# Performance work log

Measured on AMD Instinct MI355X. Metric: run time of the kernel, lower is better.

## Reference

```python
import jax, jax.numpy as jnp
import numpy as np

D_MODEL = 1024
N_HEADS = 16
KV_HEADS = 4
D_HEAD = D_MODEL // N_HEADS


def _rope_factor(n, d_head, dtype):
    # theta = 10000 ** (-2*(i//2)/d_head); buffers cos/sin = outer(pos, theta)
    # then sin[1::2] (odd positions) negated. Module applies q*cos + q*sin,
    # i.e. elementwise scale by (cos + sin_mod) -- faithful to the source.
    i = jnp.arange(d_head)
    theta = jnp.power(jnp.asarray(10000.0, dtype), (-2.0 * (i // 2) / d_head).astype(dtype))
    pos = jnp.arange(n, dtype=dtype)
    ang = pos[:, None] * theta[None, :]          # [n, d_head]
    sign = jnp.where(jnp.arange(n) % 2 == 1, -1.0, 1.0).astype(dtype)
    return jnp.cos(ang) + sign[:, None] * jnp.sin(ang)  # [n, d_head]


def _rms_norm(x, g):
    eps = jnp.finfo(x.dtype).eps  # torch nn.RMSNorm(eps=None) default
    inv = jax.lax.rsqrt(jnp.mean(x * x, axis=-1, keepdims=True) + eps)
    return x * inv * g


def setup_inputs() -> dict:
    key = jax.random.key(0)
    ks = jax.random.split(key, 5)
    s_in = 1.0 / np.sqrt(D_MODEL)
    x = jax.random.normal(ks[0], (2, 2048, D_MODEL), dtype=jnp.float32)
    # weights stored [in, out] (apply as x @ W)
    w_q = jax.random.normal(ks[1], (D_MODEL, D_MODEL), dtype=jnp.float32) * s_in
    w_k = jax.random.normal(ks[2], (D_MODEL, D_HEAD * KV_HEADS), dtype=jnp.float32) * s_in
    w_v = jax.random.normal(ks[3], (D_MODEL, D_HEAD * KV_HEADS), dtype=jnp.float32) * s_in
    w_o = jax.random.normal(ks[4], (D_MODEL, D_MODEL), dtype=jnp.float32) * s_in
    g = jnp.ones((D_MODEL,), dtype=jnp.float32)  # RMSNorm weight
    return {"x": x, "w_q": w_q, "w_k": w_k, "w_v": w_v, "w_o": w_o, "g": g}


def reference(x, w_q, w_k, w_v, w_o, g):
    b, n, _ = x.shape
    reps = N_HEADS // KV_HEADS
    x_norm = _rms_norm(x, g)
    q = (x_norm @ w_q).reshape(b, n, N_HEADS, D_HEAD).transpose(0, 2, 1, 3)   # [b,h,n,a]
    k = (x_norm @ w_k).reshape(b, n, KV_HEADS, D_HEAD).transpose(0, 2, 1, 3)  # [b,k,n,a]
    v = (x_norm @ w_v).reshape(b, n, KV_HEADS, D_HEAD).transpose(0, 2, 1, 3)
    rf = _rope_factor(n, D_HEAD, x.dtype)  # [n, a]
    q = q * rf
    k = k * rf
    # GQA: k.repeat(1, reps, 1, 1) tiles heads -> q head h pairs with kv head h % KV_HEADS.
    # Avoid materializing the tiled k/v by grouping q heads.
    q5 = q.reshape(b, reps, KV_HEADS, n, D_HEAD)
    scale = jnp.asarray(np.sqrt(D_MODEL), x.dtype)  # note: sqrt(d_model), as in source
    qkt = jnp.einsum('brkqa,bkca->brkqc', q5, k) / scale  # [b,reps,kv,n,n]
    attn = jax.nn.softmax(qkt, axis=-1)
    s = jnp.einsum('brkqc,bkca->brkqa', attn, v)           # [b,reps,kv,n,a]
    s = s.reshape(b, N_HEADS, n, D_HEAD).transpose(0, 2, 1, 3).reshape(b, n, D_MODEL)
    o = s @ w_o
    return s + o
```

## Files before the change

### kernel.cpp

```cpp
#include <hip/hip_runtime.h>
#include <hip/hip_bf16.h>

typedef short bf16x8 __attribute__((ext_vector_type(8)));
typedef float f32x4 __attribute__((ext_vector_type(4)));

#define MFMA16(a, b, c) __builtin_amdgcn_mfma_f32_16x16x32_bf16((a), (b), (c), 0, 0, 0)

#define QSCALE 0.045084220027780106f

static __device__ __forceinline__ unsigned short f2bf_bits(float f) {
    union { float f; unsigned u; } v; v.f = f;
    unsigned u = v.u;
    u += 0x7fff + ((u >> 16) & 1);
    return (unsigned short)(u >> 16);
}
static __device__ __forceinline__ unsigned pk_trunc(float lo, float hi) {
    union { float f; unsigned u; } a, b; a.f = lo; b.f = hi;
    return __builtin_amdgcn_perm(b.u, a.u, 0x07060302);
}
static __device__ __forceinline__ void load_lds16(const void* g, void* s) {
    __builtin_amdgcn_global_load_lds(
        (const __attribute__((address_space(1))) unsigned int*)g,
        (__attribute__((address_space(3))) unsigned int*)s, 16, 0, 0);
}
static __device__ __forceinline__ size_t gemm_swz(int row, int k, int ld) {
    return (size_t)row * ld + (k & ~31) + ((((k >> 3) & 3) ^ (row & 3)) * 8) + (k & 7);
}
static __device__ __forceinline__ size_t k_swz(int key, int feat) {
    return (size_t)(key >> 5) * 2048 + (size_t)(((((key >> 4) & 1) * 2) + (feat >> 5)) * 512)
         + (key & 15) * 32 + ((feat >> 3) & 3) * 8 + (feat & 7);
}
static __device__ __forceinline__ size_t v_swz(int key, int feat) {
    return (size_t)(key >> 5) * 2048 + (size_t)((feat >> 4) * 512)
         + (feat & 15) * 32 + ((key >> 3) & 3) * 8 + (key & 7);
}

__global__ __launch_bounds__(256) void prep_kernel(
    const float* __restrict__ x, const float* __restrict__ w_q,
    const float* __restrict__ w_k, const float* __restrict__ w_v,
    const float* __restrict__ w_o, const float* __restrict__ g,
    __hip_bfloat16* __restrict__ xn, __hip_bfloat16* __restrict__ wqkv,
    __hip_bfloat16* __restrict__ wo_t, float* __restrict__ rope)
{
    __shared__ float tile[32][33];
    __shared__ float red[4];
    const int blk = blockIdx.x, tid = threadIdx.x;

    if (blk >= 3072) {
        const int row = blk - 3072;
        const float4 xv = ((const float4*)(x + (size_t)row * 1024))[tid];
        float ss = xv.x * xv.x + xv.y * xv.y + xv.z * xv.z + xv.w * xv.w;
        #pragma unroll
        for (int m = 32; m; m >>= 1) ss += __shfl_xor(ss, m);
        if ((tid & 63) == 0) red[tid >> 6] = ss;
        __syncthreads();
        const float tot = red[0] + red[1] + red[2] + red[3];
        const float inv = rsqrtf(tot * (1.0f / 1024.0f) + 1.1920928955078125e-07f);
        const float4 gv = ((const float4*)g)[tid];
        ushort4 o;
        o.x = f2bf_bits(xv.x * inv * gv.x);
        o.y = f2bf_bits(xv.y * inv * gv.y);
        o.z = f2bf_bits(xv.z * inv * gv.z);
        o.w = f2bf_bits(xv.w * inv * gv.w);
        *(ushort4*)&xn[gemm_swz(row, tid * 4, 1024)] = o;
        return;
    }
    if (blk >= 2560) {
        const int idx = (blk - 2560) * 256 + tid;
        const int pos = idx >> 6, i = idx & 63;
        const float theta = powf(10000.0f, -2.0f * (float)(i >> 1) / 64.0f);
        const float ang = (float)pos * theta;
        const float sgn = (pos & 1) ? -1.0f : 1.0f;
        rope[idx] = cosf(ang) + sgn * sinf(ang);
        return;
    }
    const float* src; __hip_bfloat16* dst; int C, i0;
    if (blk < 1024)      { src = w_q; dst = wqkv;                     C = 1024; i0 = blk; }
    else if (blk < 1280) { src = w_k; dst = wqkv + (size_t)1024*1024; C = 256;  i0 = blk - 1024; }
    else if (blk < 1536) { src = w_v; dst = wqkv + (size_t)1280*1024; C = 256;  i0 = blk - 1280; }
    else                 { src = w_o; dst = wo_t;                     C = 1024; i0 = blk - 1536; }
    const int tpr = C >> 5;
    const int c0 = (i0 % tpr) * 32, r0 = (i0 / tpr) * 32;
    const int tx = tid & 31, ty = tid >> 5;
    #pragma unroll
    for (int j = 0; j < 4; j++) {
        int i = ty + j * 8;
        tile[i][tx] = src[(size_t)(r0 + i) * C + c0 + tx];
    }
    __syncthreads();
    #pragma unroll
    for (int j = 0; j < 4; j++) {
        int i = ty + j * 8;
        dst[gemm_swz(c0 + i, r0 + tx, 1024)] = __float2bfloat16(tile[tx][i]);
    }
}

template <int MODE>
__global__ __launch_bounds__(256, 3) void gemm_kernel(
    const __hip_bfloat16* __restrict__ Abf, const __hip_bfloat16* __restrict__ Bt,
    int M, int N, int K,
    const float* __restrict__ rope,
    __hip_bfloat16* __restrict__ q_bf, __hip_bfloat16* __restrict__ k_bf,
    __hip_bfloat16* __restrict__ vt_bf,
    const __hip_bfloat16* __restrict__ s_in, float* __restrict__ out)
{
    __shared__ __hip_bfloat16 As[2][64 * 32];
    __shared__ __hip_bfloat16 Bs[2][128 * 32];
    const int tid = threadIdx.x;
    const int wv = tid >> 6, lane = tid & 63, quad = lane >> 4, l16 = lane & 15;
    const int m0 = blockIdx.y * 64, n0 = blockIdx.x * 128;
    const int Kt = K >> 5;
    const int rw = lane >> 2, ch = lane & 3;

    f32x4 acc[4][2] = {};

    load_lds16(&Abf[(size_t)(m0 + wv * 16 + rw) * K + ch * 8], &As[0][wv * 512]);
    #pragma unroll
    for (int j = 0; j < 2; j++) {
        const int bi = wv * 2 + j;
        load_lds16(&Bt[(size_t)(n0 + bi * 16 + rw) * K + ch * 8], &Bs[0][bi * 512]);
    }

    for (int t = 0; t < Kt; t++) {
        __syncthreads();
        if (t + 1 < Kt) {
            const int k0 = (t + 1) * 32, nb = (t + 1) & 1;
            load_lds16(&Abf[(size_t)(m0 + wv * 16 + rw) * K + k0 + ch * 8], &As[nb][wv * 512]);
            #pragma unroll
            for (int j = 0; j < 2; j++) {
                const int bi = wv * 2 + j;
                load_lds16(&Bt[(size_t)(n0 + bi * 16 + rw) * K + k0 + ch * 8], &Bs[nb][bi * 512]);
            }
        }
        const __hip_bfloat16* Ab = As[t & 1];
        const __hip_bfloat16* Bb = Bs[t & 1];
        const int csw = (quad ^ (l16 & 3)) * 8;
        bf16x8 af[4], bfr[2];
        #pragma unroll
        for (int i = 0; i < 4; i++) af[i] = *(const bf16x8*)&Ab[(i * 16 + l16) * 32 + csw];
        #pragma unroll
        for (int n = 0; n < 2; n++) bfr[n] = *(const bf16x8*)&Bb[(wv * 32 + n * 16 + l16) * 32 + csw];
        #pragma unroll
        for (int mt = 0; mt < 4; mt++)
            #pragma unroll
            for (int nt = 0; nt < 2; nt++)
                acc[mt][nt] = MFMA16(af[mt], bfr[nt], acc[mt][nt]);
    }

    #pragma unroll
    for (int mt = 0; mt < 4; mt++) {
        #pragma unroll
        for (int nt = 0; nt < 2; nt++) {
            const int gn = n0 + wv * 32 + nt * 16 + l16;
            #pragma unroll
            for (int r = 0; r < 4; r++) {
                const int m = m0 + mt * 16 + quad * 4 + r;
                float val = acc[mt][nt][r];
                if (MODE == 0) {
                    const int bb = m >> 11, pos = m & 2047;
                    const int a = gn & 63;
                    if (gn < 1024) {
                        const int hh = gn >> 6;
                        val *= rope[pos * 64 + a] * QSCALE;
                        q_bf[((((size_t)bb * 16 + hh) * 2048) + pos) * 64 + a] = __float2bfloat16(val);
                    } else if (gn < 1280) {
                        const int kvh = (gn - 1024) >> 6;
                        val *= rope[pos * 64 + a];
                        k_bf[((size_t)bb * 4 + kvh) * 131072 + k_swz(pos, a)] = __float2bfloat16(val);
                    } else {
                        const int kvh = (gn - 1280) >> 6;
                        vt_bf[((size_t)bb * 4 + kvh) * 131072 + v_swz(pos, a)] = __float2bfloat16(val);
                    }
                } else {
                    out[(size_t)m * N + gn] = val + __bfloat162float(s_in[gemm_swz(m, gn, 1024)]);
                }
            }
        }
    }
}

#define ATTN_STEP(T, KC, KN, PWOFF, PROFF)                                          \
    {                                                                               \
        f32x4 sc[2][4] = {};                                                        \
        _Pragma("unroll") for (int ks = 0; ks < 2; ks++)                            \
            _Pragma("unroll") for (int nt = 0; nt < 2; nt++)                        \
                _Pragma("unroll") for (int qt = 0; qt < 4; qt++)                    \
                    sc[nt][qt] = MFMA16(KC[nt * 2 + ks], bq[qt][ks], sc[nt][qt]);   \
        if ((T) > 0) {                                                              \
            _Pragma("unroll") for (int i = 0; i < 4; i++)                           \
                va[i] = *(const bf16x8*)&Vp[(size_t)((T) - 1) * 2048 + i * 512];    \
        }                                                                           \
        if ((T) < 31) {                                                             \
            _Pragma("unroll") for (int i = 0; i < 4; i++)                           \
                KN[i] = *(const bf16x8*)&Kp[(size_t)((T) + 1) * 2048 + i * 512];    \
        }                                                                           \
        {                                                                           \
            __hip_bfloat16* P = Pw + (PWOFF);                                       \
            _Pragma("unroll") for (int nt = 0; nt < 2; nt++)                        \
                _Pragma("unroll") for (int qt = 0; qt < 4; qt++) {                  \
                    const float e0 = __builtin_amdgcn_exp2f(sc[nt][qt][0]);         \
                    const float e1 = __builtin_amdgcn_exp2f(sc[nt][qt][1]);         \
                    const float e2 = __builtin_amdgcn_exp2f(sc[nt][qt][2]);         \
                    const float e3 = __builtin_amdgcn_exp2f(sc[nt][qt][3]);         \
                    uint2 pk;                                                       \
                    pk.x = pk_trunc(e0, e1);                                        \
                    pk.y = pk_trunc(e2, e3);                                        \
                    *(uint2*)&P[(qt * 16 + l16) * 40 + nt * 16 + quad * 4] = pk;    \
                }                                                                   \
        }                                                                           \
        if ((T) > 0) {                                                              \
            const __hip_bfloat16* P = Pw + (PROFF);                                 \
            _Pragma("unroll") for (int qt = 0; qt < 4; qt++) {                      \
                bf16x8 bp = *(const bf16x8*)&P[(qt * 16 + l16) * 40 + quad * 8];    \
                _Pragma("unroll") for (int ft = 0; ft < 4; ft++)                    \
                    oacc[ft][qt] = MFMA16(va[ft], bp, oacc[ft][qt]);                \
                lacc[qt] = MFMA16(ones, bp, lacc[qt]);                              \
            }                                                                       \
        }                                                                           \
    }

__global__ __launch_bounds__(512, 2) void attn_kernel(
    const __hip_bfloat16* __restrict__ q_bf, const __hip_bfloat16* __restrict__ k_bf,
    const __hip_bfloat16* __restrict__ vt_bf, __hip_bfloat16* __restrict__ s_bf)
{
    __shared__ char smem[81920];
    const int tid = threadIdx.x;
    const int wv = tid >> 6, lane = tid & 63, quad = lane >> 4, l16 = lane & 15;
    const int wl = wv & 3, sp = wv >> 2;
    const int qtile = blockIdx.x, bh = blockIdx.y;
    const int b = bh >> 4, h = bh & 15, kvh = h & 3;
    const int q0 = qtile * 256 + wl * 64;

    const __hip_bfloat16* Qp = q_bf + ((((size_t)b * 16 + h) * 2048) + q0) * 64;
    const __hip_bfloat16* Kp = k_bf + ((size_t)b * 4 + kvh) * 131072 + (size_t)sp * 65536 + l16 * 32 + quad * 8;
    const __hip_bfloat16* Vp = vt_bf + ((size_t)b * 4 + kvh) * 131072 + (size_t)sp * 65536 + l16 * 32 + quad * 8;
    __hip_bfloat16* Pw = (__hip_bfloat16*)(smem + wv * 10240);

    bf16x8 bq[4][2];
    #pragma unroll
    for (int qt = 0; qt < 4; qt++)
        #pragma unroll
        for (int ks = 0; ks < 2; ks++)
            bq[qt][ks] = *(const bf16x8*)&Qp[(size_t)(qt * 16 + l16) * 64 + ks * 32 + quad * 8];

    bf16x8 ones;
    #pragma unroll
    for (int i = 0; i < 8; i++) ones[i] = (short)0x3F80;

    bf16x8 ka0[4], ka1[4], va[4];
    #pragma unroll
    for (int i = 0; i < 4; i++) ka0[i] = *(const bf16x8*)&Kp[i * 512];

    f32x4 oacc[4][4] = {};
    f32x4 lacc[4] = {};

    for (int tt = 0; tt < 16; tt++) {
        const int t0 = tt * 2;
        ATTN_STEP(t0,     ka0, ka1, 0,    2560)
        ATTN_STEP(t0 + 1, ka1, ka0, 2560, 0)
    }
    #pragma unroll
    for (int i = 0; i < 4; i++)
        va[i] = *(const bf16x8*)&Vp[(size_t)31 * 2048 + i * 512];
    {
        const __hip_bfloat16* P = Pw + 2560;
        #pragma unroll
        for (int qt = 0; qt < 4; qt++) {
            bf16x8 bp = *(const bf16x8*)&P[(qt * 16 + l16) * 40 + quad * 8];
            #pragma unroll
            for (int ft = 0; ft < 4; ft++)
                oacc[ft][qt] = MFMA16(va[ft], bp, oacc[ft][qt]);
            lacc[qt] = MFMA16(ones, bp, lacc[qt]);
        }
    }

    float* exch = (float*)(smem) + wl * 4352;
    float* lex  = (float*)(smem + 69632) + wl * 64;
    __syncthreads();
    if (sp == 1) {
        #pragma unroll
        for (int qt = 0; qt < 4; qt++) {
            #pragma unroll
            for (int ft = 0; ft < 4; ft++)
                *(float4*)&exch[(qt * 16 + l16) * 68 + ft * 16 + quad * 4] = *(const float4*)&oacc[ft][qt];
            if (quad == 0) lex[qt * 16 + l16] = lacc[qt][0];
        }
    }
    __syncthreads();
    if (sp == 0) {
        #pragma unroll
        for (int qt = 0; qt < 4; qt++) {
            const float inv = 1.0f / (lacc[qt][0] + lex[qt * 16 + l16]);
            const int row = (b * 2048) + q0 + qt * 16 + l16;
            #pragma unroll
            for (int ft = 0; ft < 4; ft++) {
                const float4 up = *(const float4*)&exch[(qt * 16 + l16) * 68 + ft * 16 + quad * 4];
                const int feat = h * 64 + ft * 16 + quad * 4;
                ushort4 o;
                o.x = f2bf_bits((oacc[ft][qt][0] + up.x) * inv);
                o.y = f2bf_bits((oacc[ft][qt][1] + up.y) * inv);
                o.z = f2bf_bits((oacc[ft][qt][2] + up.z) * inv);
                o.w = f2bf_bits((oacc[ft][qt][3] + up.w) * inv);
                *(ushort4*)&s_bf[gemm_swz(row, feat, 1024)] = o;
            }
        }
    }
}

extern "C" void kernel_launch(void* const* d_in, const int* in_sizes, int n_in,
                              void* d_out, int out_size, void* d_ws, size_t ws_size,
                              hipStream_t stream)
{
    (void)in_sizes; (void)n_in; (void)out_size; (void)ws_size;
    const float* x   = (const float*)d_in[0];
    const float* w_q = (const float*)d_in[1];
    const float* w_k = (const float*)d_in[2];
    const float* w_v = (const float*)d_in[3];
    const float* w_o = (const float*)d_in[4];
    const float* g   = (const float*)d_in[5];
    float* out = (float*)d_out;

    char* p = (char*)d_ws;
    __hip_bfloat16* xn    = (__hip_bfloat16*)p; p += (size_t)4096 * 1024 * 2;
    __hip_bfloat16* wqkv  = (__hip_bfloat16*)p; p += (size_t)1536 * 1024 * 2;
    __hip_bfloat16* wo_t  = (__hip_bfloat16*)p; p += (size_t)1024 * 1024 * 2;
    float*          rope  = (float*)p;          p += (size_t)2048 * 64 * 4;
    __hip_bfloat16* q_bf  = (__hip_bfloat16*)p; p += (size_t)2 * 16 * 2048 * 64 * 2;
    __hip_bfloat16* k_bf  = (__hip_bfloat16*)p; p += (size_t)2 * 4 * 2048 * 64 * 2;
    __hip_bfloat16* vt_bf = (__hip_bfloat16*)p; p += (size_t)2 * 4 * 64 * 2048 * 2;
    __hip_bfloat16* s_bf  = (__hip_bfloat16*)p; p += (size_t)4096 * 1024 * 2;

    prep_kernel<<<7168, 256, 0, stream>>>(x, w_q, w_k, w_v, w_o, g, xn, wqkv, wo_t, rope);
    gemm_kernel<0><<<dim3(12, 64), 256, 0, stream>>>(xn, wqkv, 4096, 1536, 1024,
                                                     rope, q_bf, k_bf, vt_bf, nullptr, nullptr);
    attn_kernel<<<dim3(8, 32), 512, 0, stream>>>(q_bf, k_bf, vt_bf, s_bf);
    gemm_kernel<1><<<dim3(8, 64), 256, 0, stream>>>(s_bf, wo_t, 4096, 1024, 1024,
                                                    nullptr, nullptr, nullptr, nullptr, s_bf, out);
}
```

Baseline: 176.6 us.

## Double GEMM K-tile to 64 and prefetch attention V a step earlier

The GEMM kernel now stages 64-wide K slices per iteration instead of 32, widening the LDS swizzle to 8 chunks and running two MFMA sub-steps per barrier. This halves the number of barrier and DMA rounds but doubles LDS use per block, which could limit occupancy. The attention kernel double-buffers V registers so V for step T is loaded during step T, one step before it is consumed, hiding load latency at the cost of more VGPRs. The swizzle change in gemm_swz also alters how the prep kernel writes its layout.

```diff
diff --git a/kernel.cpp b/kernel.cpp
--- a/kernel.cpp
+++ b/kernel.cpp
@@ -24,7 +24,7 @@
         (__attribute__((address_space(3))) unsigned int*)s, 16, 0, 0);
 }
 static __device__ __forceinline__ size_t gemm_swz(int row, int k, int ld) {
-    return (size_t)row * ld + (k & ~31) + ((((k >> 3) & 3) ^ (row & 3)) * 8) + (k & 7);
+    return (size_t)row * ld + (k & ~63) + ((((k >> 3) & 7) ^ (row & 7)) * 8) + (k & 7);
 }
 static __device__ __forceinline__ size_t k_swz(int key, int feat) {
     return (size_t)(key >> 5) * 2048 + (size_t)(((((key >> 4) & 1) * 2) + (feat >> 5)) * 512)
@@ -104,47 +104,48 @@
     __hip_bfloat16* __restrict__ vt_bf,
     const __hip_bfloat16* __restrict__ s_in, float* __restrict__ out)
 {
-    __shared__ __hip_bfloat16 As[2][64 * 32];
-    __shared__ __hip_bfloat16 Bs[2][128 * 32];
+    __shared__ __hip_bfloat16 As[2][64 * 64];
+    __shared__ __hip_bfloat16 Bs[2][128 * 64];
     const int tid = threadIdx.x;
     const int wv = tid >> 6, lane = tid & 63, quad = lane >> 4, l16 = lane & 15;
     const int m0 = blockIdx.y * 64, n0 = blockIdx.x * 128;
-    const int Kt = K >> 5;
-    const int rw = lane >> 2, ch = lane & 3;
+    const int Kt = K >> 6;
+    const int rw = lane >> 3, ch = lane & 7;
 
     f32x4 acc[4][2] = {};
 
-    load_lds16(&Abf[(size_t)(m0 + wv * 16 + rw) * K + ch * 8], &As[0][wv * 512]);
-    #pragma unroll
-    for (int j = 0; j < 2; j++) {
-        const int bi = wv * 2 + j;
-        load_lds16(&Bt[(size_t)(n0 + bi * 16 + rw) * K + ch * 8], &Bs[0][bi * 512]);
-    }
+    #define GEMM_DMA(BUF, K0)                                                        \
+        _Pragma("unroll") for (int j = 0; j < 2; j++)                                \
+            load_lds16(&Abf[(size_t)(m0 + wv * 16 + j * 8 + rw) * K + (K0) + ch * 8],\
+                       &As[BUF][(wv * 16 + j * 8) * 64]);                            \
+        _Pragma("unroll") for (int j = 0; j < 4; j++)                                \
+            load_lds16(&Bt[(size_t)(n0 + wv * 32 + j * 8 + rw) * K + (K0) + ch * 8], \
+                       &Bs[BUF][(wv * 32 + j * 8) * 64]);
+
+    GEMM_DMA(0, 0)
 
     for (int t = 0; t < Kt; t++) {
         __syncthreads();
         if (t + 1 < Kt) {
-            const int k0 = (t + 1) * 32, nb = (t + 1) & 1;
-            load_lds16(&Abf[(size_t)(m0 + wv * 16 + rw) * K + k0 + ch * 8], &As[nb][wv * 512]);
-            #pragma unroll
-            for (int j = 0; j < 2; j++) {
-                const int bi = wv * 2 + j;
-                load_lds16(&Bt[(size_t)(n0 + bi * 16 + rw) * K + k0 + ch * 8], &Bs[nb][bi * 512]);
-            }
+            const int nb = (t + 1) & 1, k0 = (t + 1) * 64;
+            GEMM_DMA(nb, k0)
         }
         const __hip_bfloat16* Ab = As[t & 1];
         const __hip_bfloat16* Bb = Bs[t & 1];
-        const int csw = (quad ^ (l16 & 3)) * 8;
-        bf16x8 af[4], bfr[2];
-        #pragma unroll
-        for (int i = 0; i < 4; i++) af[i] = *(const bf16x8*)&Ab[(i * 16 + l16) * 32 + csw];
-        #pragma unroll
-        for (int n = 0; n < 2; n++) bfr[n] = *(const bf16x8*)&Bb[(wv * 32 + n * 16 + l16) * 32 + csw];
-        #pragma unroll
-        for (int mt = 0; mt < 4; mt++)
-            #pragma unroll
-            for (int nt = 0; nt < 2; nt++)
-                acc[mt][nt] = MFMA16(af[mt], bfr[nt], acc[mt][nt]);
+        #pragma unroll
+        for (int ks = 0; ks < 2; ks++) {
+            const int pos = ((ks * 4 + quad) ^ (l16 & 7)) * 8;
+            bf16x8 af[4], bfr[2];
+            #pragma unroll
+            for (int i = 0; i < 4; i++) af[i] = *(const bf16x8*)&Ab[(i * 16 + l16) * 64 + pos];
+            #pragma unroll
+            for (int n = 0; n < 2; n++) bfr[n] = *(const bf16x8*)&Bb[(wv * 32 + n * 16 + l16) * 64 + pos];
+            #pragma unroll
+            for (int mt = 0; mt < 4; mt++)
+                #pragma unroll
+                for (int nt = 0; nt < 2; nt++)
+                    acc[mt][nt] = MFMA16(af[mt], bfr[nt], acc[mt][nt]);
+        }
     }
 
     #pragma unroll
@@ -179,17 +180,15 @@
     }
 }
 
-#define ATTN_STEP(T, KC, KN, PWOFF, PROFF)                                          \
+#define ATTN_STEP(T, KC, KN, VC, VN, PWOFF, PROFF)                                  \
     {                                                                               \
         f32x4 sc[2][4] = {};                                                        \
         _Pragma("unroll") for (int ks = 0; ks < 2; ks++)                            \
             _Pragma("unroll") for (int nt = 0; nt < 2; nt++)                        \
                 _Pragma("unroll") for (int qt = 0; qt < 4; qt++)                    \
                     sc[nt][qt] = MFMA16(KC[nt * 2 + ks], bq[qt][ks], sc[nt][qt]);   \
-        if ((T) > 0) {                                                              \
-            _Pragma("unroll") for (int i = 0; i < 4; i++)                           \
-                va[i] = *(const bf16x8*)&Vp[(size_t)((T) - 1) * 2048 + i * 512];    \
-        }                                                                           \
+        _Pragma("unroll") for (int i = 0; i < 4; i++)                               \
+            VN[i] = *(const bf16x8*)&Vp[(size_t)(T) * 2048 + i * 512];              \
         if ((T) < 31) {                                                             \
             _Pragma("unroll") for (int i = 0; i < 4; i++)                           \
                 KN[i] = *(const bf16x8*)&Kp[(size_t)((T) + 1) * 2048 + i * 512];    \
@@ -213,7 +212,7 @@
             _Pragma("unroll") for (int qt = 0; qt < 4; qt++) {                      \
                 bf16x8 bp = *(const bf16x8*)&P[(qt * 16 + l16) * 40 + quad * 8];    \
                 _Pragma("unroll") for (int ft = 0; ft < 4; ft++)                    \
-                    oacc[ft][qt] = MFMA16(va[ft], bp, oacc[ft][qt]);                \
+                    oacc[ft][qt] = MFMA16(VC[ft], bp, oacc[ft][qt]);                \
                 lacc[qt] = MFMA16(ones, bp, lacc[qt]);                              \
             }                                                                       \
         }                                                                           \
@@ -247,7 +246,7 @@
     #pragma unroll
     for (int i = 0; i < 8; i++) ones[i] = (short)0x3F80;
 
-    bf16x8 ka0[4], ka1[4], va[4];
+    bf16x8 ka0[4], ka1[4], va0[4], va1[4];
     #pragma unroll
     for (int i = 0; i < 4; i++) ka0[i] = *(const bf16x8*)&Kp[i * 512];
 
@@ -256,12 +255,9 @@
 
     for (int tt = 0; tt < 16; tt++) {
         const int t0 = tt * 2;
-        ATTN_STEP(t0,     ka0, ka1, 0,    2560)
-        ATTN_STEP(t0 + 1, ka1, ka0, 2560, 0)
-    }
-    #pragma unroll
-    for (int i = 0; i < 4; i++)
-        va[i] = *(const bf16x8*)&Vp[(size_t)31 * 2048 + i * 512];
+        ATTN_STEP(t0,     ka0, ka1, va1, va0, 0,    2560)
+        ATTN_STEP(t0 + 1, ka1, ka0, va0, va1, 2560, 0)
+    }
     {
         const __hip_bfloat16* P = Pw + 2560;
         #pragma unroll
@@ -269,7 +265,7 @@
             bf16x8 bp = *(const bf16x8*)&P[(qt * 16 + l16) * 40 + quad * 8];
             #pragma unroll
             for (int ft = 0; ft < 4; ft++)
-                oacc[ft][qt] = MFMA16(va[ft], bp, oacc[ft][qt]);
+                oacc[ft][qt] = MFMA16(va1[ft], bp, oacc[ft][qt]);
             lacc[qt] = MFMA16(ones, bp, lacc[qt]);
         }
     }
```

Measured after the change: 164.9 us. 6.6% less time.
